# Optimization experiments

Hardware: AMD Instinct MI355X
Metric: run time of the kernel (lower is better)

Reference implementation:

```python
import jax, jax.numpy as jnp
import numpy as np

B, T, I, H = 512, 128, 128, 512


def setup_inputs() -> dict:
    key = jax.random.key(0)
    ks = jax.random.split(key, 10)
    scale = 1.0 / np.sqrt(I + H)
    return {
        "s_inputs": jax.random.normal(ks[0], (B, T, I), jnp.float32),
        "l_inputs": jax.random.normal(ks[1], (B, T, I), jnp.float32),
        "dow": jax.random.randint(ks[2], (B,), 0, 7),
        "hour": jax.random.randint(ks[3], (B,), 0, 24),
        # gate weights stacked as [f, i, o, C] along output dim (math-equivalent
        # to 4 separate nn.Linear(input_size+hidden_size, hidden_size))
        "s_W": jax.random.uniform(ks[4], (I + H, 4 * H), jnp.float32, -scale, scale),
        "s_b": jax.random.uniform(ks[5], (4 * H,), jnp.float32, -scale, scale),
        "l_W": jax.random.uniform(ks[6], (I + H, 4 * H), jnp.float32, -scale, scale),
        "l_b": jax.random.uniform(ks[7], (4 * H,), jnp.float32, -scale, scale),
        "out_W": jax.random.uniform(ks[8], (2 * H, H), jnp.float32, -1.0 / np.sqrt(2 * H), 1.0 / np.sqrt(2 * H)),
        "out_b": jax.random.uniform(ks[9], (H,), jnp.float32, -1.0 / np.sqrt(2 * H), 1.0 / np.sqrt(2 * H)),
    }


def _cell(x, h, c, W, b):
    # one LSTM step: fused 4-gate GEMM then elementwise gate math
    g = jnp.concatenate([x, h], axis=1) @ W + b  # [B, 4H]
    f, i, o, cand = jnp.split(g, 4, axis=1)
    c_new = jax.nn.sigmoid(f) * c + jax.nn.sigmoid(i) * jnp.tanh(cand)
    h_new = jax.nn.sigmoid(o) * jnp.tanh(c_new)
    return h_new, c_new


def reference(s_inputs, l_inputs, dow, hour, s_W, s_b, l_W, l_b, out_W, out_b):
    batch = s_inputs.shape[0]
    hdim = out_b.shape[0]
    init = (jnp.zeros((batch, hdim), s_inputs.dtype),) * 4  # (sh, sc, lh, lc)

    def step(carry, xs):
        sh, sc, lh, lc = carry
        x_s, x_l = xs
        sh, sc = _cell(x_s, sh, sc, s_W, s_b)
        lh, lc = _cell(x_l, lh, lc, l_W, l_b)
        return (sh, sc, lh, lc), None

    xs = (jnp.swapaxes(s_inputs, 0, 1), jnp.swapaxes(l_inputs, 0, 1))  # [T,B,I]
    (sh, _, lh, _), _ = jax.lax.scan(step, init, xs)
    return jnp.tanh(jnp.concatenate([sh, lh], axis=1) @ out_W + out_b)
```

## Files before the change

### kernel.cpp

```cpp
#include <hip/hip_runtime.h>

#define HD 512
#define KD 640
#define G4 2048

typedef short short8 __attribute__((ext_vector_type(8)));
typedef __bf16 bf16x8 __attribute__((ext_vector_type(8)));
typedef float floatx4 __attribute__((ext_vector_type(4)));
typedef unsigned int uintx4 __attribute__((ext_vector_type(4)));

static __device__ __forceinline__ unsigned short f2bf(float f) {
  unsigned int u = __float_as_uint(f);
  u += 0x7fffu + ((u >> 16) & 1u);
  return (unsigned short)(u >> 16);
}
static __device__ __forceinline__ float rcp_(float x) {
  return __builtin_amdgcn_rcpf(x);
}
static __device__ __forceinline__ float sigmoidf_(float x) {
  return rcp_(1.f + __expf(-x));
}
static __device__ __forceinline__ float tanhf_(float x) {
  float ax = fabsf(x);
  float e = __expf(-2.f * ax);
  float r = fmaf(-2.f * e, rcp_(1.f + e), 1.f);
  return copysignf(r, x);
}
static __device__ __forceinline__ uintx4 load16_cc(unsigned long long a) {
  uintx4 r;
  asm volatile("global_load_dwordx4 %0, %1, off sc0 sc1" : "=v"(r) : "v"(a) : "memory");
  return r;
}
static __device__ __forceinline__ void store16_cc(unsigned long long a, uintx4 v) {
  asm volatile("global_store_dwordx4 %0, %1, off sc0 sc1" :: "v"(a), "v"(v) : "memory");
}
static __device__ __forceinline__ void waitcnt_vm0() {
  asm volatile("s_waitcnt vmcnt(0)" ::: "memory");
}

__global__ __launch_bounds__(256) void transpose_f32_bf16(
    const float* __restrict__ src, unsigned short* __restrict__ dst,
    int R, int C) {
  __shared__ unsigned short tile[64][80];
  int nR = R >> 6;
  int tr = blockIdx.x % nR;
  int tc = blockIdx.x / nR;
  int tid = threadIdx.x;
#pragma unroll
  for (int i = 0; i < 2; ++i) {
    int seg = tid + i * 256;
    int row = seg >> 3, ks8 = (seg & 7) * 8;
    const float* p = src + (size_t)(tr * 64 + row) * C + tc * 64 + ks8;
    short8 v;
#pragma unroll
    for (int q = 0; q < 8; ++q) v[q] = (short)f2bf(p[q]);
    *(short8*)(&tile[row][ks8]) = v;
  }
  __syncthreads();
#pragma unroll
  for (int i = 0; i < 2; ++i) {
    int seg = tid + i * 256;
    int cl = seg >> 3, rs8 = (seg & 7) * 8;
    short8 v;
#pragma unroll
    for (int q = 0; q < 8; ++q) v[q] = (short)tile[rs8 + q][cl];
    *(short8*)(dst + (size_t)(tc * 64 + cl) * R + tr * 64 + rs8) = v;
  }
}

__global__ __launch_bounds__(256) void xconv(
    const float* __restrict__ xs, const float* __restrict__ xl,
    unsigned short* __restrict__ xTs, unsigned short* __restrict__ xTl) {
  int t = blockIdx.x & 127;
  int bc = (blockIdx.x >> 7) & 3;
  int which = blockIdx.x >> 9;
  const float* x = which ? xl : xs;
  unsigned short* xT = which ? xTl : xTs;
  int b0 = bc * 128;
#pragma unroll
  for (int i = 0; i < 8; ++i) {
    int seg = threadIdx.x + i * 256;
    int bl_ = seg >> 4, i8 = (seg & 15) * 8;
    const float* p = x + (size_t)(b0 + bl_) * 16384 + t * 128 + i8;
    short8 v;
#pragma unroll
    for (int q = 0; q < 8; ++q) v[q] = (short)f2bf(p[q]);
    *(short8*)(xT + ((size_t)t * 512 + b0 + bl_) * 128 + i8) = v;
  }
}

__global__ __launch_bounds__(256, 1) void lstm_persistent(
    const unsigned short* __restrict__ xTs, const unsigned short* __restrict__ xTl,
    const unsigned short* __restrict__ WTs, const unsigned short* __restrict__ WTl,
    const float* __restrict__ bs, const float* __restrict__ bl,
    unsigned short* __restrict__ hs0, unsigned short* __restrict__ hs1,
    unsigned short* __restrict__ hl0, unsigned short* __restrict__ hl1,
    int* __restrict__ flags) {
  const int bid = blockIdx.x;
  const int lstm = bid & 1;
  const int mb = (bid >> 1) & 15;
  const int nb = bid >> 5;
  const int grp = lstm * 16 + mb;
  const int b0 = mb * 32;
  const int H0 = nb * 64;

  const unsigned short* xT = lstm ? xTl : xTs;
  const unsigned short* WT = lstm ? WTl : WTs;
  const float* bias = lstm ? bl : bs;
  unsigned short* h0 = lstm ? hl0 : hs0;
  unsigned short* h1 = lstm ? hl1 : hs1;

  __shared__ unsigned short As[32][648];
  __shared__ unsigned short hbuf[32][72];

  const int tid = threadIdx.x;
  const int wn = tid >> 6;
  const int lane = tid & 63;
  const int quad = lane >> 4;
  const int lrow = lane & 15;
  const int colL = wn * 16 + lrow;

  float bias_r[4];
#pragma unroll
  for (int g = 0; g < 4; ++g) bias_r[g] = bias[g * HD + H0 + colL];
  float c_r[8];
#pragma unroll
  for (int j = 0; j < 8; ++j) c_r[j] = 0.f;

  bf16x8 breg[4][20];
#pragma unroll
  for (int g = 0; g < 4; ++g) {
    const unsigned short* wp = WT + (size_t)(g * HD + H0 + colL) * KD + quad * 8;
#pragma unroll
    for (int kc = 0; kc < 20; ++kc)
      breg[g][kc] = __builtin_bit_cast(bf16x8, *(const short8*)(wp + kc * 32));
  }

  const int st_row = tid >> 3, st_c8 = (tid & 7) * 8;
  const unsigned long long hstA =
      (unsigned long long)(h1 + (size_t)(b0 + st_row) * HD + H0 + st_c8);
  const unsigned long long hstB =
      (unsigned long long)(h0 + (size_t)(b0 + st_row) * HD + H0 + st_c8);

#pragma unroll 1
  for (int t = 0; t < 128; ++t) {
    const unsigned short* hr = (t & 1) ? h1 : h0;

#pragma unroll
    for (int i = 0; i < 2; ++i) {
      int seg = tid + i * 256;
      int row = seg >> 4, ch = seg & 15;
      short8 v = *(const short8*)(xT + ((size_t)t * 512 + b0 + row) * 128 + ch * 8);
      *(short8*)(&As[row][ch * 8]) = v;
    }

    if (t > 0) {
      if (wn == 0) {
        while (true) {
          int v = __hip_atomic_load(flags + grp * 16 + (lane & 7),
                                    __ATOMIC_RELAXED, __HIP_MEMORY_SCOPE_AGENT);
          if (__ballot(v >= t) == 0xFFFFFFFFFFFFFFFFull) break;
          __builtin_amdgcn_s_sleep(1);
        }
      }
      __syncthreads();
      uintx4 hv_[8];
#pragma unroll
      for (int i = 0; i < 8; ++i) {
        int chunk = tid + i * 256;
        int row = chunk >> 6, ch = chunk & 63;
        hv_[i] = load16_cc((unsigned long long)(hr + (size_t)(b0 + row) * HD + ch * 8));
      }
      waitcnt_vm0();
#pragma unroll
      for (int i = 0; i < 8; ++i) {
        int chunk = tid + i * 256;
        int row = chunk >> 6, ch = chunk & 63;
        *(uintx4*)(&As[row][128 + ch * 8]) = hv_[i];
      }
    } else {
#pragma unroll
      for (int i = 0; i < 8; ++i) {
        int chunk = tid + i * 256;
        int row = chunk >> 6, ch = chunk & 63;
        *(uintx4*)(&As[row][128 + ch * 8]) = (uintx4){0, 0, 0, 0};
      }
    }
    __syncthreads();

    floatx4 acc[2][4];
#pragma unroll
    for (int mt = 0; mt < 2; ++mt)
#pragma unroll
      for (int g = 0; g < 4; ++g) acc[mt][g] = (floatx4){0.f, 0.f, 0.f, 0.f};
#pragma unroll
    for (int kc = 0; kc < 20; ++kc) {
      bf16x8 a0 = __builtin_bit_cast(bf16x8, *(const short8*)(&As[lrow][kc * 32 + quad * 8]));
      bf16x8 a1 = __builtin_bit_cast(bf16x8, *(const short8*)(&As[16 + lrow][kc * 32 + quad * 8]));
#pragma unroll
      for (int g = 0; g < 4; ++g) {
        acc[0][g] = __builtin_amdgcn_mfma_f32_16x16x32_bf16(a0, breg[g][kc], acc[0][g], 0, 0, 0);
        acc[1][g] = __builtin_amdgcn_mfma_f32_16x16x32_bf16(a1, breg[g][kc], acc[1][g], 0, 0, 0);
      }
    }

#pragma unroll
    for (int mt = 0; mt < 2; ++mt)
#pragma unroll
      for (int r = 0; r < 4; ++r) {
        int j = mt * 4 + r;
        float fg = acc[mt][0][r] + bias_r[0];
        float ig = acc[mt][1][r] + bias_r[1];
        float og = acc[mt][2][r] + bias_r[2];
        float cg = acc[mt][3][r] + bias_r[3];
        float cn = sigmoidf_(fg) * c_r[j] + sigmoidf_(ig) * tanhf_(cg);
        float hn = sigmoidf_(og) * tanhf_(cn);
        c_r[j] = cn;
        hbuf[mt * 16 + quad * 4 + r][colL] = f2bf(hn);
      }
    __syncthreads();

    {
      short8 hv8 = *(const short8*)(&hbuf[st_row][st_c8]);
      store16_cc((t & 1) ? hstB : hstA, __builtin_bit_cast(uintx4, hv8));
      waitcnt_vm0();
    }
    __syncthreads();

    if (tid == 0 && t < 127)
      __hip_atomic_store(flags + grp * 16 + nb, t + 1,
                         __ATOMIC_RELAXED, __HIP_MEMORY_SCOPE_AGENT);
  }
}

__global__ __launch_bounds__(256) void out_gemm(
    const unsigned short* __restrict__ hs, const unsigned short* __restrict__ hl,
    const unsigned short* __restrict__ WTo,
    const float* __restrict__ ob, float* __restrict__ out) {
  const int bx = blockIdx.x;
  const int mb = bx & 7;
  const int nb = bx >> 3;

  __shared__ unsigned short As2[64][88];
  __shared__ unsigned short Bs2[128][88];

  const int tid = threadIdx.x;
  const int wave = tid >> 6;
  const int lane = tid & 63;
  const int quad = lane >> 4;
  const int lrow = lane & 15;
  const int wm = wave & 1;
  const int wn = wave >> 1;

  floatx4 acc[8];
#pragma unroll
  for (int i = 0; i < 8; ++i) acc[i] = (floatx4){0.f, 0.f, 0.f, 0.f};

  for (int k0 = 0; k0 < 1024; k0 += 64) {
#pragma unroll
    for (int i = 0; i < 2; ++i) {
      int seg = tid + i * 256;
      int row = seg >> 3, ks8 = (seg & 7) * 8;
      int kg = k0 + ks8;
      int b = mb * 64 + row;
      const unsigned short* src =
          (kg < 512) ? (hs + (size_t)b * HD + kg) : (hl + (size_t)b * HD + (kg - 512));
      *(short8*)(&As2[row][ks8]) = *(const short8*)src;
    }
#pragma unroll
    for (int i = 0; i < 4; ++i) {
      int seg = tid + i * 256;
      int n = seg >> 3, ks8 = (seg & 7) * 8;
      *(short8*)(&Bs2[n][ks8]) =
          *(const short8*)(WTo + (size_t)(nb * 128 + n) * 1024 + k0 + ks8);
    }
    __syncthreads();
#pragma unroll
    for (int ks = 0; ks < 64; ks += 32) {
      int kq = ks + quad * 8;
      bf16x8 a0 = __builtin_bit_cast(bf16x8, *(const short8*)(&As2[wm * 32 + lrow][kq]));
      bf16x8 a1 = __builtin_bit_cast(bf16x8, *(const short8*)(&As2[wm * 32 + 16 + lrow][kq]));
#pragma unroll
      for (int nt = 0; nt < 4; ++nt) {
        bf16x8 bfr = __builtin_bit_cast(bf16x8, *(const short8*)(&Bs2[wn * 64 + nt * 16 + lrow][kq]));
        acc[nt] = __builtin_amdgcn_mfma_f32_16x16x32_bf16(a0, bfr, acc[nt], 0, 0, 0);
        acc[4 + nt] = __builtin_amdgcn_mfma_f32_16x16x32_bf16(a1, bfr, acc[4 + nt], 0, 0, 0);
      }
    }
    __syncthreads();
  }
#pragma unroll
  for (int mt = 0; mt < 2; ++mt) {
#pragma unroll
    for (int nt = 0; nt < 4; ++nt) {
      int n = nb * 128 + wn * 64 + nt * 16 + lrow;
      float bv = ob[n];
#pragma unroll
      for (int r = 0; r < 4; ++r) {
        int b = mb * 64 + wm * 32 + mt * 16 + quad * 4 + r;
        out[(size_t)b * HD + n] = tanhf_(acc[mt * 4 + nt][r] + bv);
      }
    }
  }
}

extern "C" void kernel_launch(void* const* d_in, const int* in_sizes, int n_in,
                              void* d_out, int out_size, void* d_ws, size_t ws_size,
                              hipStream_t stream) {
  (void)in_sizes; (void)n_in; (void)out_size; (void)ws_size;
  const float* xs = (const float*)d_in[0];
  const float* xl = (const float*)d_in[1];
  const float* sW = (const float*)d_in[4];
  const float* sb = (const float*)d_in[5];
  const float* lW = (const float*)d_in[6];
  const float* lb = (const float*)d_in[7];
  const float* oW = (const float*)d_in[8];
  const float* ob = (const float*)d_in[9];

  char* w = (char*)d_ws;
  int* flags = (int*)w;
  unsigned short* WTs = (unsigned short*)(w + 4096);
  unsigned short* WTl = WTs + (size_t)G4 * KD;
  unsigned short* WTo = WTl + (size_t)G4 * KD;
  unsigned short* xTs = WTo + (size_t)HD * 1024;
  unsigned short* xTl = xTs + (size_t)128 * 512 * 128;
  unsigned short* hs0 = xTl + (size_t)128 * 512 * 128;
  unsigned short* hs1 = hs0 + (size_t)512 * HD;
  unsigned short* hl0 = hs1 + (size_t)512 * HD;
  unsigned short* hl1 = hl0 + (size_t)512 * HD;

  hipMemsetAsync(flags, 0, 4096, stream);
  transpose_f32_bf16<<<(640 / 64) * (2048 / 64), 256, 0, stream>>>(sW, WTs, 640, 2048);
  transpose_f32_bf16<<<(640 / 64) * (2048 / 64), 256, 0, stream>>>(lW, WTl, 640, 2048);
  transpose_f32_bf16<<<(1024 / 64) * (512 / 64), 256, 0, stream>>>(oW, WTo, 1024, 512);
  xconv<<<1024, 256, 0, stream>>>(xs, xl, xTs, xTl);

  const float* sbp = sb; const float* lbp = lb;
  const unsigned short *xTs_c = xTs, *xTl_c = xTl, *WTs_c = WTs, *WTl_c = WTl;
  unsigned short *a_hs0 = hs0, *a_hs1 = hs1, *a_hl0 = hl0, *a_hl1 = hl1;
  int* a_flags = flags;
  void* args[] = {(void*)&xTs_c, (void*)&xTl_c, (void*)&WTs_c, (void*)&WTl_c,
                  (void*)&sbp, (void*)&lbp, (void*)&a_hs0, (void*)&a_hs1,
                  (void*)&a_hl0, (void*)&a_hl1, (void*)&a_flags};
  hipError_t e = hipLaunchCooperativeKernel((const void*)lstm_persistent,
                                            dim3(256), dim3(256), args, 0, stream);
  if (e != hipSuccess) {
    lstm_persistent<<<256, 256, 0, stream>>>(xTs, xTl, WTs, WTl, sb, lb,
                                             hs0, hs1, hl0, hl1, flags);
  }
  out_gemm<<<32, 256, 0, stream>>>(hs0, hl0, WTo, ob, (float*)d_out);
}
```

Measured before the change: 858.7 us.

## Overlap recurrent h load with input-part MFMAs via direct-to-LDS loads

Recurrent h values are now loaded with global_load_lds straight into shared memory instead of going through registers. The first four K-chunks, which cover only the x input, are computed while those loads are in flight. The next timestep's x slice is prefetched after the h store, and the store wait, x prefetch and flag publish are merged, which removes one barrier per step. This shortens the serialized critical path of each recurrent step. The risk is memory-ordering subtleties: x is written into As after the step with no trailing barrier, and the flag is set after only thread 0's own waitcnt.

```diff
diff --git a/kernel.cpp b/kernel.cpp
--- a/kernel.cpp
+++ b/kernel.cpp
@@ -26,16 +26,16 @@
   float r = fmaf(-2.f * e, rcp_(1.f + e), 1.f);
   return copysignf(r, x);
 }
-static __device__ __forceinline__ uintx4 load16_cc(unsigned long long a) {
-  uintx4 r;
-  asm volatile("global_load_dwordx4 %0, %1, off sc0 sc1" : "=v"(r) : "v"(a) : "memory");
-  return r;
-}
 static __device__ __forceinline__ void store16_cc(unsigned long long a, uintx4 v) {
   asm volatile("global_store_dwordx4 %0, %1, off sc0 sc1" :: "v"(a), "v"(v) : "memory");
 }
 static __device__ __forceinline__ void waitcnt_vm0() {
   asm volatile("s_waitcnt vmcnt(0)" ::: "memory");
+}
+static __device__ __forceinline__ void load_lds16_cc(const void* g, void* l) {
+  __builtin_amdgcn_global_load_lds(
+      (const __attribute__((address_space(1))) void*)(unsigned long long)(uintptr_t)g,
+      (__attribute__((address_space(3))) void*)l, 16, 0, 17);
 }
 
 __global__ __launch_bounds__(256) void transpose_f32_bf16(
@@ -142,51 +142,41 @@
   const unsigned long long hstB =
       (unsigned long long)(h0 + (size_t)(b0 + st_row) * HD + H0 + st_c8);
 
+#pragma unroll
+  for (int i = 0; i < 2; ++i) {
+    int seg = tid + i * 256;
+    int row = seg >> 4, ch = seg & 15;
+    short8 v = *(const short8*)(xT + ((size_t)(b0 + row)) * 128 + ch * 8);
+    *(short8*)(&As[row][ch * 8]) = v;
+  }
+#pragma unroll
+  for (int i = 0; i < 8; ++i) {
+    int chunk = tid + i * 256;
+    int row = chunk >> 6, ch = chunk & 63;
+    *(uintx4*)(&As[row][128 + ch * 8]) = (uintx4){0, 0, 0, 0};
+  }
+
 #pragma unroll 1
   for (int t = 0; t < 128; ++t) {
     const unsigned short* hr = (t & 1) ? h1 : h0;
 
-#pragma unroll
-    for (int i = 0; i < 2; ++i) {
-      int seg = tid + i * 256;
-      int row = seg >> 4, ch = seg & 15;
-      short8 v = *(const short8*)(xT + ((size_t)t * 512 + b0 + row) * 128 + ch * 8);
-      *(short8*)(&As[row][ch * 8]) = v;
-    }
+    if (t > 0 && wn == 0) {
+      while (true) {
+        int v = __hip_atomic_load(flags + grp * 16 + (lane & 7),
+                                  __ATOMIC_RELAXED, __HIP_MEMORY_SCOPE_AGENT);
+        if (__ballot(v >= t) == 0xFFFFFFFFFFFFFFFFull) break;
+        __builtin_amdgcn_s_sleep(1);
+      }
+    }
+    __syncthreads();
 
     if (t > 0) {
-      if (wn == 0) {
-        while (true) {
-          int v = __hip_atomic_load(flags + grp * 16 + (lane & 7),
-                                    __ATOMIC_RELAXED, __HIP_MEMORY_SCOPE_AGENT);
-          if (__ballot(v >= t) == 0xFFFFFFFFFFFFFFFFull) break;
-          __builtin_amdgcn_s_sleep(1);
-        }
-      }
-      __syncthreads();
-      uintx4 hv_[8];
 #pragma unroll
       for (int i = 0; i < 8; ++i) {
-        int chunk = tid + i * 256;
-        int row = chunk >> 6, ch = chunk & 63;
-        hv_[i] = load16_cc((unsigned long long)(hr + (size_t)(b0 + row) * HD + ch * 8));
-      }
-      waitcnt_vm0();
-#pragma unroll
-      for (int i = 0; i < 8; ++i) {
-        int chunk = tid + i * 256;
-        int row = chunk >> 6, ch = chunk & 63;
-        *(uintx4*)(&As[row][128 + ch * 8]) = hv_[i];
-      }
-    } else {
-#pragma unroll
-      for (int i = 0; i < 8; ++i) {
-        int chunk = tid + i * 256;
-        int row = chunk >> 6, ch = chunk & 63;
-        *(uintx4*)(&As[row][128 + ch * 8]) = (uintx4){0, 0, 0, 0};
-      }
-    }
-    __syncthreads();
+        int row = wn + i * 4;
+        load_lds16_cc(hr + (size_t)(b0 + row) * HD + lane * 8, &As[row][128]);
+      }
+    }
 
     floatx4 acc[2][4];
 #pragma unroll
@@ -194,7 +184,21 @@
 #pragma unroll
       for (int g = 0; g < 4; ++g) acc[mt][g] = (floatx4){0.f, 0.f, 0.f, 0.f};
 #pragma unroll
-    for (int kc = 0; kc < 20; ++kc) {
+    for (int kc = 0; kc < 4; ++kc) {
+      bf16x8 a0 = __builtin_bit_cast(bf16x8, *(const short8*)(&As[lrow][kc * 32 + quad * 8]));
+      bf16x8 a1 = __builtin_bit_cast(bf16x8, *(const short8*)(&As[16 + lrow][kc * 32 + quad * 8]));
+#pragma unroll
+      for (int g = 0; g < 4; ++g) {
+        acc[0][g] = __builtin_amdgcn_mfma_f32_16x16x32_bf16(a0, breg[g][kc], acc[0][g], 0, 0, 0);
+        acc[1][g] = __builtin_amdgcn_mfma_f32_16x16x32_bf16(a1, breg[g][kc], acc[1][g], 0, 0, 0);
+      }
+    }
+
+    waitcnt_vm0();
+    __syncthreads();
+
+#pragma unroll
+    for (int kc = 4; kc < 20; ++kc) {
       bf16x8 a0 = __builtin_bit_cast(bf16x8, *(const short8*)(&As[lrow][kc * 32 + quad * 8]));
       bf16x8 a1 = __builtin_bit_cast(bf16x8, *(const short8*)(&As[16 + lrow][kc * 32 + quad * 8]));
 #pragma unroll
@@ -220,16 +224,30 @@
       }
     __syncthreads();
 
-    {
-      short8 hv8 = *(const short8*)(&hbuf[st_row][st_c8]);
-      store16_cc((t & 1) ? hstB : hstA, __builtin_bit_cast(uintx4, hv8));
-      waitcnt_vm0();
-    }
-    __syncthreads();
-
-    if (tid == 0 && t < 127)
-      __hip_atomic_store(flags + grp * 16 + nb, t + 1,
-                         __ATOMIC_RELAXED, __HIP_MEMORY_SCOPE_AGENT);
+    short8 hv8 = *(const short8*)(&hbuf[st_row][st_c8]);
+    store16_cc((t & 1) ? hstB : hstA, __builtin_bit_cast(uintx4, hv8));
+
+    short8 xv[2];
+    if (t < 127) {
+#pragma unroll
+      for (int i = 0; i < 2; ++i) {
+        int seg = tid + i * 256;
+        int row = seg >> 4, ch = seg & 15;
+        xv[i] = *(const short8*)(xT + ((size_t)(t + 1) * 512 + b0 + row) * 128 + ch * 8);
+      }
+    }
+    waitcnt_vm0();
+    if (t < 127) {
+#pragma unroll
+      for (int i = 0; i < 2; ++i) {
+        int seg = tid + i * 256;
+        int row = seg >> 4, ch = seg & 15;
+        *(short8*)(&As[row][ch * 8]) = xv[i];
+      }
+      if (tid == 0)
+        __hip_atomic_store(flags + grp * 16 + nb, t + 1,
+                           __ATOMIC_RELAXED, __HIP_MEMORY_SCOPE_AGENT);
+    }
   }
 }
 
```

After: 741.5 us. 13.6% less time.
